# Performance work log

Hardware: AMD Instinct MI355X
Metric: run time of the kernel (lower is better)

## Reference

```python
import jax, jax.numpy as jnp
import numpy as np

MIN_NORM = 1e-15
BALL_EPS = 0.004  # torch.float32 entry of BALL_EPS
SCALING = float(np.tanh(1.0 / 2.0))  # tanh(tau/2), tau=1.0
N_GRAPHS = 512
BN_EPS = 1e-5


def _cmin(v):
    return jnp.maximum(v, MIN_NORM)


def project(x):
    norm = _cmin(jnp.linalg.norm(x, axis=-1, keepdims=True))
    maxnorm = 1.0 - BALL_EPS
    return jnp.where(norm > maxnorm, x / norm * maxnorm, x)


def isometric_transform(x, a):
    r2 = jnp.sum(a * a, axis=-1, keepdims=True) - 1.0
    u = x - a
    return r2 / _cmin(jnp.sum(u * u, axis=-1, keepdims=True)) * u + a


def reflect_at_zero(x, mu):
    a = mu / _cmin(jnp.sum(mu * mu, axis=-1, keepdims=True))
    return isometric_transform(x, a)


def reflect_through_zero(p, q, x):
    p_ = p / _cmin(jnp.linalg.norm(p, axis=-1, keepdims=True))
    q_ = q / _cmin(jnp.linalg.norm(q, axis=-1, keepdims=True))
    r = q_ - p_
    m = jnp.sum(r * x, axis=-1, keepdims=True) / jnp.sum(r * r, axis=-1, keepdims=True)
    return x - 2.0 * r * m


def logmap0(y):
    yn = _cmin(jnp.linalg.norm(y, axis=-1, keepdims=True))
    return y / yn * jnp.arctanh(jnp.clip(yn, -1.0 + 1e-15, 1.0 - 1e-15))


def unique_rows(m):
    # Emulates torch.unique(dim=0, return_inverse=True) for all-distinct rows
    # (true w.p. 1 for continuous activations): lexicographic sort, col 0 primary.
    n = m.shape[0]
    perm = jnp.lexsort(m.T[::-1])
    inv = jnp.zeros(n, jnp.int32).at[perm].set(jnp.arange(n, dtype=jnp.int32))
    return m[perm], inv


def _forward(x, edge_index, batch, W0, b0, convW1, convb1, gamma, beta, convW2,
             convb2, fc1W, fc1b, fc2W, fc2b, fc3W, fc3b):
    n = x.shape[0]
    d = W0.shape[1]
    x = jax.nn.relu(x @ W0 + b0)
    xs = [x]
    z = [jnp.zeros((1, d), x.dtype)]
    inv = [jnp.zeros(n, jnp.int32)]
    u, iv = unique_rows(jax.lax.stop_gradient(x))  # no_grad in original
    z.append(SCALING * project(u))
    inv.append(iv)
    src, dst = edge_index[0], edge_index[1]
    n_layers = convW1.shape[0]
    p_vec = jnp.zeros((d,), x.dtype).at[-1].set(1.0)
    for i in range(n_layers):
        # GINConv (eps=0): MLP(x + sum_{j->i} x_j)
        agg = jax.ops.segment_sum(x[src], dst, num_segments=n)
        h = x + agg
        h = jax.nn.relu(h @ convW1[i] + convb1[i])
        mu = jnp.mean(h, axis=0)
        var = jnp.var(h, axis=0)  # biased, as BatchNorm1d training mode
        h = gamma[i] * (h - mu) / jnp.sqrt(var + BN_EPS) + beta[i]
        x = jax.nn.relu(h @ convW2[i] + convb2[i])
        x = x.at[:, -1].set(0.0)  # x @ diag zeroes last column
        xs.append(x)
        u_full, iv = unique_rows(jax.lax.stop_gradient(jnp.concatenate(xs, axis=1)))
        cnt = jax.ops.segment_sum(jnp.ones(n, jnp.int32), iv, num_segments=n)
        u = u_full[:, -d:]
        z_children = SCALING * project(u)
        t1 = jax.ops.segment_sum(inv[i + 1], iv, num_segments=n) // cnt
        z_current = z[i + 1][t1]
        t2 = jax.ops.segment_sum(inv[i], iv, num_segments=n) // cnt
        z_parent = z[i][t2]
        z_parent = reflect_at_zero(z_parent, z_current)
        z_children = reflect_through_zero(z_parent, p_vec, z_children)
        z_all = reflect_at_zero(z_children, z_current)
        inv.append(iv)
        z.append(z_all)
    xh = logmap0(z[-1])[inv[-1]]
    out = jax.ops.segment_sum(xh, batch, num_segments=N_GRAPHS)
    out = jax.nn.relu(out @ fc1W + fc1b)
    out = jax.nn.relu(out @ fc2W + fc2b)
    out = out @ fc3W + fc3b
    return jax.nn.log_softmax(out, axis=1)


def setup_inputs() -> dict:
    N, E, D_IN, D, L, C = 50000, 800000, 128, 64, 3, 10
    key = jax.random.key(0)
    ks = jax.random.split(key, 12)
    s = 0.05
    return {
        "x": jax.random.normal(ks[0], (N, D_IN), jnp.float32),
        "edge_index": jax.random.randint(ks[1], (2, E), 0, N),
        "batch": jnp.sort(jax.random.randint(ks[2], (N,), 0, 512)),
        "W0": jax.random.normal(ks[3], (D_IN, D), jnp.float32) * s,
        "b0": jnp.zeros((D,), jnp.float32),
        "convW1": jax.random.normal(ks[4], (L, D, D), jnp.float32) * s,
        "convb1": jnp.zeros((L, D), jnp.float32),
        "gamma": jnp.ones((L, D), jnp.float32),
        "beta": jnp.zeros((L, D), jnp.float32),
        "convW2": jax.random.normal(ks[5], (L, D, D), jnp.float32) * s,
        "convb2": jnp.zeros((L, D), jnp.float32),
        "fc1W": jax.random.normal(ks[6], (D, 128), jnp.float32) * s,
        "fc1b": jnp.zeros((128,), jnp.float32),
        "fc2W": jax.random.normal(ks[7], (128, 64), jnp.float32) * s,
        "fc2b": jnp.zeros((64,), jnp.float32),
        "fc3W": jax.random.normal(ks[8], (64, C), jnp.float32) * s,
        "fc3b": jnp.zeros((C,), jnp.float32),
    }


def reference(x, edge_index, batch, W0, b0, convW1, convb1, gamma, beta, convW2,
              convb2, fc1W, fc1b, fc2W, fc2b, fc3W, fc3b):
    return _forward(x, edge_index, batch, W0, b0, convW1, convb1, gamma, beta,
                    convW2, convb2, fc1W, fc1b, fc2W, fc2b, fc3W, fc3b)
```

## Files before the change

### kernel.cpp

```cpp
#include <hip/hip_runtime.h>
#include <hip/hip_fp16.h>
#include <math.h>

#define SCALING_F 0.46211715726000974f
#define MAXNORM_F 0.996f
#define MINNORM_F 1e-15f
#define BN_EPS_F  1e-5f

#define NBUCKET 32

typedef _Float16 v8h __attribute__((ext_vector_type(8)));
typedef float    v4f __attribute__((ext_vector_type(4)));

__device__ __forceinline__ float rsum16(float v) {
  v += __shfl_xor(v, 1, 64);
  v += __shfl_xor(v, 2, 64);
  v += __shfl_xor(v, 4, 64);
  v += __shfl_xor(v, 8, 64);
  return v;
}

__device__ __forceinline__ void rsum16x6(float& a, float& b, float& c,
                                         float& d, float& e, float& f) {
#pragma unroll
  for (int o = 1; o <= 8; o <<= 1) {
    a += __shfl_xor(a, o, 64);
    b += __shfl_xor(b, o, 64);
    c += __shfl_xor(c, o, 64);
    d += __shfl_xor(d, o, 64);
    e += __shfl_xor(e, o, 64);
    f += __shfl_xor(f, o, 64);
  }
}

__device__ __forceinline__ float h2f(float v) {
  return __half2float(__float2half(v));
}

__device__ __forceinline__ void acc8(float* a, uint4 u) {
  __half2 h0 = *(__half2*)&u.x;
  __half2 h1 = *(__half2*)&u.y;
  __half2 h2 = *(__half2*)&u.z;
  __half2 h3 = *(__half2*)&u.w;
  a[0] += __low2float(h0); a[1] += __high2float(h0);
  a[2] += __low2float(h1); a[3] += __high2float(h1);
  a[4] += __low2float(h2); a[5] += __high2float(h2);
  a[6] += __low2float(h3); a[7] += __high2float(h3);
}

__device__ __forceinline__ void load4f(const __half* p, float* a) {
  uint2 u = *(const uint2*)p;
  __half2 h0 = *(__half2*)&u.x;
  __half2 h1 = *(__half2*)&u.y;
  a[0] = __low2float(h0); a[1] = __high2float(h0);
  a[2] = __low2float(h1); a[3] = __high2float(h1);
}

__global__ __launch_bounds__(256) void k_wcvt(
    const float* __restrict__ W0, const float* __restrict__ cW1,
    const float* __restrict__ cW2, int L,
    __half* __restrict__ W0T, __half* __restrict__ W1T, __half* __restrict__ W2T)
{
  int id = blockIdx.x * 256 + threadIdx.x;
  if (id < 64 * 128) {
    int n = id >> 7, k = id & 127;
    W0T[id] = __float2half(W0[(size_t)k * 64 + n]);
  }
  if (id < L * 64 * 64) {
    int l = id >> 12, rem = id & 4095;
    int n = rem >> 6, k = rem & 63;
    W1T[id] = __float2half(cW1[(size_t)l * 4096 + k * 64 + n]);
    W2T[id] = __float2half(cW2[(size_t)l * 4096 + k * 64 + n]);
  }
}

__global__ __launch_bounds__(256) void k_gb(const int* __restrict__ batch,
                                            int N, int G, int* __restrict__ gstart)
{
  int r = blockIdx.x * 256 + threadIdx.x;
  if (r >= N) return;
  int b = batch[r];
  int prev = (r == 0) ? -1 : batch[r - 1];
  for (int g = prev + 1; g <= b; ++g) gstart[g] = r;
  if (r == N - 1)
    for (int g = b + 1; g <= G; ++g) gstart[g] = N;
}

__global__ __launch_bounds__(256) void k_mm0(
    const float* __restrict__ A, const __half* __restrict__ BT,
    const float* __restrict__ bias, __half* __restrict__ X, int M)
{
  const int tid  = threadIdx.x;
  const int w    = tid >> 6;
  const int lane = tid & 63;
  const int q    = lane >> 4;
  const int i    = lane & 15;
  const int rblk = blockIdx.x * 64;
  const int arow = rblk + w * 16 + i;

  v4f acc[4];
#pragma unroll
  for (int t = 0; t < 4; ++t) acc[t] = (v4f){0.f, 0.f, 0.f, 0.f};

#pragma unroll
  for (int hh = 0; hh < 4; ++hh) {
    v8h af = (v8h){0, 0, 0, 0, 0, 0, 0, 0};
    if (arow < M) {
      const float* p = &A[(size_t)arow * 128 + hh * 32 + q * 8];
      float4 fa = *(const float4*)p;
      float4 fb = *(const float4*)(p + 4);
      af[0] = (_Float16)fa.x; af[1] = (_Float16)fa.y;
      af[2] = (_Float16)fa.z; af[3] = (_Float16)fa.w;
      af[4] = (_Float16)fb.x; af[5] = (_Float16)fb.y;
      af[6] = (_Float16)fb.z; af[7] = (_Float16)fb.w;
    }
#pragma unroll
    for (int t = 0; t < 4; ++t) {
      v8h bf = *(const v8h*)&BT[(size_t)(t * 16 + i) * 128 + hh * 32 + q * 8];
      acc[t] = __builtin_amdgcn_mfma_f32_16x16x32_f16(af, bf, acc[t], 0, 0, 0);
    }
  }

#pragma unroll
  for (int j = 0; j < 4; ++j) {
    int row = rblk + w * 16 + 4 * q + j;
    if (row >= M) continue;
#pragma unroll
    for (int t = 0; t < 4; ++t)
      X[(size_t)row * 64 + i + 16 * t] =
          __float2half(fmaxf(acc[t][j] + bias[i + 16 * t], 0.f));
  }
}

__global__ __launch_bounds__(256, 6) void k_layer1(
    const __half* __restrict__ x, const int* __restrict__ rowptr,
    const unsigned short* __restrict__ csr, const __half* __restrict__ BT,
    const float* __restrict__ bias, __half* __restrict__ h,
    float* __restrict__ gstatP, int M)
{
  __shared__ __half AsH[16][80];
  const int tid  = threadIdx.x;
  const int w    = tid >> 6;
  const int lane = tid & 63;
  const int q    = lane >> 4;
  const int i    = lane & 15;
  const int g8   = lane >> 3;
  const int i8   = lane & 7;
  const int rblk = blockIdx.x * 16;

  const int r0 = rblk + w * 4 + 0;
  const int r1 = rblk + w * 4 + 1;
  const int r2 = rblk + w * 4 + 2;
  const int r3 = rblk + w * 4 + 3;
  const bool v0 = (r0 < M), v1 = (r1 < M), v2 = (r2 < M), v3 = (r3 < M);

  float a0[8] = {0.f,0.f,0.f,0.f,0.f,0.f,0.f,0.f};
  float a1[8] = {0.f,0.f,0.f,0.f,0.f,0.f,0.f,0.f};
  float a2[8] = {0.f,0.f,0.f,0.f,0.f,0.f,0.f,0.f};
  float a3[8] = {0.f,0.f,0.f,0.f,0.f,0.f,0.f,0.f};

  int c0 = 0, e0 = 0, c1 = 0, e1 = 0, c2 = 0, e2 = 0, c3 = 0, e3 = 0;
  if (v0) { c0 = rowptr[r0]; e0 = rowptr[r0 + 1]; }
  if (v1) { c1 = rowptr[r1]; e1 = rowptr[r1 + 1]; }
  if (v2) { c2 = rowptr[r2]; e2 = rowptr[r2 + 1]; }
  if (v3) { c3 = rowptr[r3]; e3 = rowptr[r3 + 1]; }

  if (v0 && g8 == 0) acc8(a0, *(const uint4*)&x[(size_t)r0 * 64 + 8 * i8]);
  if (v1 && g8 == 0) acc8(a1, *(const uint4*)&x[(size_t)r1 * 64 + 8 * i8]);
  if (v2 && g8 == 0) acc8(a2, *(const uint4*)&x[(size_t)r2 * 64 + 8 * i8]);
  if (v3 && g8 == 0) acc8(a3, *(const uint4*)&x[(size_t)r3 * 64 + 8 * i8]);

  while ((c0 + 8 <= e0) | (c1 + 8 <= e1) | (c2 + 8 <= e2) | (c3 + 8 <= e3)) {
    const bool d0 = (c0 + 8 <= e0);
    const bool d1 = (c1 + 8 <= e1);
    const bool d2 = (c2 + 8 <= e2);
    const bool d3 = (c3 + 8 <= e3);
    int n0 = 0, n1 = 0, n2 = 0, n3 = 0;
    if (d0) n0 = csr[c0 + g8];
    if (d1) n1 = csr[c1 + g8];
    if (d2) n2 = csr[c2 + g8];
    if (d3) n3 = csr[c3 + g8];
    uint4 u0, u1, u2, u3;
    if (d0) u0 = *(const uint4*)&x[(size_t)n0 * 64 + 8 * i8];
    if (d1) u1 = *(const uint4*)&x[(size_t)n1 * 64 + 8 * i8];
    if (d2) u2 = *(const uint4*)&x[(size_t)n2 * 64 + 8 * i8];
    if (d3) u3 = *(const uint4*)&x[(size_t)n3 * 64 + 8 * i8];
    if (d0) { acc8(a0, u0); c0 += 8; }
    if (d1) { acc8(a1, u1); c1 += 8; }
    if (d2) { acc8(a2, u2); c2 += 8; }
    if (d3) { acc8(a3, u3); c3 += 8; }
  }
  {
    const int rem0 = e0 - c0;
    const int rem1 = e1 - c1;
    const int rem2 = e2 - c2;
    const int rem3 = e3 - c3;
    int n0 = 0, n1 = 0, n2 = 0, n3 = 0;
    if (g8 < rem0) n0 = csr[c0 + g8];
    if (g8 < rem1) n1 = csr[c1 + g8];
    if (g8 < rem2) n2 = csr[c2 + g8];
    if (g8 < rem3) n3 = csr[c3 + g8];
    uint4 u0, u1, u2, u3;
    if (g8 < rem0) u0 = *(const uint4*)&x[(size_t)n0 * 64 + 8 * i8];
    if (g8 < rem1) u1 = *(const uint4*)&x[(size_t)n1 * 64 + 8 * i8];
    if (g8 < rem2) u2 = *(const uint4*)&x[(size_t)n2 * 64 + 8 * i8];
    if (g8 < rem3) u3 = *(const uint4*)&x[(size_t)n3 * 64 + 8 * i8];
    if (g8 < rem0) acc8(a0, u0);
    if (g8 < rem1) acc8(a1, u1);
    if (g8 < rem2) acc8(a2, u2);
    if (g8 < rem3) acc8(a3, u3);
  }

#pragma unroll
  for (int k = 0; k < 8; ++k) {
#pragma unroll
    for (int o = 8; o <= 32; o <<= 1) {
      a0[k] += __shfl_xor(a0[k], o, 64);
      a1[k] += __shfl_xor(a1[k], o, 64);
      a2[k] += __shfl_xor(a2[k], o, 64);
      a3[k] += __shfl_xor(a3[k], o, 64);
    }
  }
  if (g8 == 0) {
    __half hv[8];
#pragma unroll
    for (int k = 0; k < 8; ++k) hv[k] = __float2half(a0[k]);
    *(uint4*)&AsH[w * 4 + 0][8 * i8] = *(uint4*)hv;
#pragma unroll
    for (int k = 0; k < 8; ++k) hv[k] = __float2half(a1[k]);
    *(uint4*)&AsH[w * 4 + 1][8 * i8] = *(uint4*)hv;
#pragma unroll
    for (int k = 0; k < 8; ++k) hv[k] = __float2half(a2[k]);
    *(uint4*)&AsH[w * 4 + 2][8 * i8] = *(uint4*)hv;
#pragma unroll
    for (int k = 0; k < 8; ++k) hv[k] = __float2half(a3[k]);
    *(uint4*)&AsH[w * 4 + 3][8 * i8] = *(uint4*)hv;
  }
  __syncthreads();

  v4f acc = (v4f){0.f, 0.f, 0.f, 0.f};
#pragma unroll
  for (int hh = 0; hh < 2; ++hh) {
    v8h af = *(const v8h*)&AsH[i][hh * 32 + q * 8];
    v8h bf = *(const v8h*)&BT[(size_t)(w * 16 + i) * 64 + hh * 32 + q * 8];
    acc = __builtin_amdgcn_mfma_f32_16x16x32_f16(af, bf, acc, 0, 0, 0);
  }

  const int col = w * 16 + i;
  float s = 0.f, qq = 0.f;
#pragma unroll
  for (int j = 0; j < 4; ++j) {
    int row = rblk + 4 * q + j;
    if (row >= M) continue;
    float v = h2f(fmaxf(acc[j] + bias[col], 0.f));
    h[(size_t)row * 64 + col] = __float2half(v);
    s += v;
    qq += v * v;
  }
  s  += __shfl_xor(s, 16, 64);  qq += __shfl_xor(qq, 16, 64);
  s  += __shfl_xor(s, 32, 64);  qq += __shfl_xor(qq, 32, 64);
  if (q == 0) {
    const int bkt = (blockIdx.x & (NBUCKET - 1)) * 128;
    atomicAdd(&gstatP[bkt + col], s);
    atomicAdd(&gstatP[bkt + 64 + col], qq);
  }
}

__global__ __launch_bounds__(256) void k_layer2(
    const __half* __restrict__ A, const __half* __restrict__ BT,
    const float* __restrict__ bias,
    const float* __restrict__ gstat, const float* __restrict__ gamma,
    const float* __restrict__ beta,
    __half* __restrict__ Xout, int M)
{
  __shared__ float scl_s[64], shf_s[64];
  __shared__ float tmp[128];
  const int tid  = threadIdx.x;
  const int w    = tid >> 6;
  const int lane = tid & 63;
  const int q    = lane >> 4;
  const int i    = lane & 15;
  const int rblk = blockIdx.x * 64;
  const int arow = rblk + w * 16 + i;

  if (tid < 128) {
    float a = 0.f;
#pragma unroll
    for (int b2 = 0; b2 < NBUCKET; ++b2) a += gstat[b2 * 128 + tid];
    tmp[tid] = a;
  }
  __syncthreads();
  if (tid < 64) {
    float mu  = tmp[tid] / (float)M;
    float var = tmp[64 + tid] / (float)M - mu * mu;
    float sv  = gamma[tid] / sqrtf(var + BN_EPS_F);
    scl_s[tid] = sv;
    shf_s[tid] = beta[tid] - mu * sv;
  }
  __syncthreads();

  v4f acc[4];
#pragma unroll
  for (int t = 0; t < 4; ++t) acc[t] = (v4f){0.f, 0.f, 0.f, 0.f};
#pragma unroll
  for (int hh = 0; hh < 2; ++hh) {
    const int k0 = hh * 32 + q * 8;
    v8h af = (v8h){0, 0, 0, 0, 0, 0, 0, 0};
    {
      float hv[8] = {0,0,0,0,0,0,0,0};
      if (arow < M) {
        uint4 u = *(const uint4*)&A[(size_t)arow * 64 + k0];
        __half2 h0 = *(__half2*)&u.x;
        __half2 h1 = *(__half2*)&u.y;
        __half2 h2 = *(__half2*)&u.z;
        __half2 h3 = *(__half2*)&u.w;
        hv[0] = __low2float(h0); hv[1] = __high2float(h0);
        hv[2] = __low2float(h1); hv[3] = __high2float(h1);
        hv[4] = __low2float(h2); hv[5] = __high2float(h2);
        hv[6] = __low2float(h3); hv[7] = __high2float(h3);
      }
#pragma unroll
      for (int k = 0; k < 8; ++k)
        af[k] = (_Float16)fmaf(hv[k], scl_s[k0 + k], shf_s[k0 + k]);
    }
#pragma unroll
    for (int t = 0; t < 4; ++t) {
      v8h bf = *(const v8h*)&BT[(size_t)(t * 16 + i) * 64 + k0];
      acc[t] = __builtin_amdgcn_mfma_f32_16x16x32_f16(af, bf, acc[t], 0, 0, 0);
    }
  }

#pragma unroll
  for (int j = 0; j < 4; ++j) {
    int row = rblk + w * 16 + 4 * q + j;
    if (row >= M) continue;
#pragma unroll
    for (int t = 0; t < 4; ++t) {
      float v = fmaxf(acc[t][j] + bias[i + 16 * t], 0.f);
      if (i == 15 && t == 3) v = 0.f;
      Xout[(size_t)row * 64 + i + 16 * t] = __float2half(v);
    }
  }
}

__global__ __launch_bounds__(256) void k_zchain(
    const __half* __restrict__ X0, const __half* __restrict__ X1,
    const __half* __restrict__ X2, const __half* __restrict__ X3,
    __half* __restrict__ Xh, int M)
{
  const int tid = threadIdx.x;
  const int i   = tid & 15;
  const int row = blockIdx.x * 16 + (tid >> 4);
  const bool valid = (row < M);

  float x0[4] = {0,0,0,0}, x1[4] = {0,0,0,0}, x2[4] = {0,0,0,0}, x3[4] = {0,0,0,0};
  if (valid) {
    load4f(&X0[(size_t)row * 64 + 4 * i], x0);
    load4f(&X1[(size_t)row * 64 + 4 * i], x1);
    load4f(&X2[(size_t)row * 64 + 4 * i], x2);
    load4f(&X3[(size_t)row * 64 + 4 * i], x3);
  }

  float zc[4], zp[4] = {0.f, 0.f, 0.f, 0.f};
  {
    float sx = rsum16(x0[0]*x0[0] + x0[1]*x0[1] + x0[2]*x0[2] + x0[3]*x0[3]);
    float norm = fmaxf(sqrtf(sx), MINNORM_F);
    float s = ((norm > MAXNORM_F) ? (MAXNORM_F / norm) : 1.0f) * SCALING_F;
#pragma unroll
    for (int e = 0; e < 4; ++e) zc[e] = x0[e] * s;
  }

  const float* Xi[3] = {x1, x2, x3};
#pragma unroll
  for (int li = 0; li < 3; ++li) {
    const float* xv = Xi[li];

    float p1 = xv[0]*xv[0] + xv[1]*xv[1] + xv[2]*xv[2] + xv[3]*xv[3];
    float p2 = zc[0]*zc[0]+zc[1]*zc[1]+zc[2]*zc[2]+zc[3]*zc[3];
    float p3 = zp[0]*zp[0]+zp[1]*zp[1]+zp[2]*zp[2]+zp[3]*zp[3];
    float p4 = zp[0]*zc[0]+zp[1]*zc[1]+zp[2]*zc[2]+zp[3]*zc[3];
    float p5 = zp[0]*xv[0]+zp[1]*xv[1]+zp[2]*xv[2]+zp[3]*xv[3];
    float p6 = zc[0]*xv[0]+zc[1]*xv[1]+zc[2]*xv[2]+zc[3]*xv[3];
    rsum16x6(p1, p2, p3, p4, p5, p6);
    float zc63 = __shfl(zc[3], 15, 16);
    float zp63 = __shfl(zp[3], 15, 16);

    float nzc2 = fmaxf(p2, MINNORM_F);
    float icz  = 1.0f / nzc2;
    float na2  = p2 * icz * icz;
    float r2   = na2 - 1.0f;
    float a63  = zc63 * icz;

    float sxn = fmaxf(sqrtf(p1), MINNORM_F);
    float sc  = ((sxn > MAXNORM_F) ? (MAXNORM_F / sxn) : 1.0f) * SCALING_F;
    float Sch2   = sc * sc * p1;
    float Szp_a  = p4 * icz;
    float Sa_ch  = sc * p6 * icz;
    float Szp_ch = sc * p5;
    float Su_a   = Szp_a - na2;
    float Su2    = p3 - 2.0f * Szp_a + na2;
    float nu2    = fmaxf(Su2, MINNORM_F);
    float t1     = r2 / nu2;
    float Szp22  = fmaxf(t1*t1*Su2 + 2.0f*t1*Su_a + na2, 0.0f);
    float npn    = fmaxf(sqrtf(Szp22), MINNORM_F);
    float ipn    = 1.0f / npn;
    float zp2_63 = t1 * (zp63 - a63) + a63;
    float Szp2ch = t1 * (Szp_ch - Sa_ch) + Sa_ch;
    float rdc    = -ipn * Szp2ch;
    float rdr    = 1.0f - 2.0f*ipn*zp2_63 + ipn*ipn*Szp22;
    float m2     = 2.0f * rdc / rdr;
    float Szp2a  = t1 * Su_a + na2;
    float Srr_a  = a63 - ipn * Szp2a;
    float Sc2a   = Sa_ch - m2 * Srr_a;
    float Sc22   = Sch2 - 2.0f*m2*rdc + m2*m2*rdr;
    float Sc2ma  = Sc22 - 2.0f*Sc2a + na2;
    float nu22   = fmaxf(Sc2ma, MINNORM_F);
    float t2     = r2 / nu22;

    float zn[4];
#pragma unroll
    for (int e = 0; e < 4; ++e) {
      float ai  = zc[e] * icz;
      float zp2 = t1 * (zp[e] - ai) + ai;
      float rri = ((i == 15 && e == 3) ? 1.0f : 0.0f) - ipn * zp2;
      float c2  = sc * xv[e] - m2 * rri;
      zn[e]     = t2 * (c2 - ai) + ai;
    }
#pragma unroll
    for (int e = 0; e < 4; ++e) { zp[e] = zc[e]; zc[e] = zn[e]; }
  }

  {
    float sz = rsum16(zc[0]*zc[0] + zc[1]*zc[1] + zc[2]*zc[2] + zc[3]*zc[3]);
    float yn  = fmaxf(sqrtf(sz), MINNORM_F);
    float t   = fminf(yn, 1.0f);
    float ath = 0.5f * logf((1.0f + t) / (1.0f - t));
    float wsc = ath / yn;
    if (valid) {
      __half hv[4];
      hv[0] = __float2half(zc[0] * wsc);
      hv[1] = __float2half(zc[1] * wsc);
      hv[2] = __float2half(zc[2] * wsc);
      hv[3] = __float2half(zc[3] * wsc);
      *(uint2*)&Xh[(size_t)row * 64 + 4 * i] = *(uint2*)hv;
    }
  }
}

__global__ __launch_bounds__(256) void k_deg(const int* __restrict__ dst, int E, int* deg) {
  int i0 = (blockIdx.x * 256 + threadIdx.x) * 4;
  if (i0 + 4 <= E) {
    int4 d = *(const int4*)&dst[i0];
    atomicAdd(&deg[d.x], 1);
    atomicAdd(&deg[d.y], 1);
    atomicAdd(&deg[d.z], 1);
    atomicAdd(&deg[d.w], 1);
  } else {
    for (int i = i0; i < E; ++i) atomicAdd(&deg[dst[i]], 1);
  }
}

__global__ __launch_bounds__(256) void k_scan1(const int* __restrict__ deg, int N,
                                               int* rowptr, int* bsum) {
  __shared__ int s[256];
  int t = threadIdx.x;
  int i = blockIdx.x * 256 + t;
  int v = (i < N) ? deg[i] : 0;
  s[t] = v;
  __syncthreads();
  for (int d = 1; d < 256; d <<= 1) {
    int add = (t >= d) ? s[t - d] : 0;
    __syncthreads();
    s[t] += add;
    __syncthreads();
  }
  if (i < N) rowptr[i] = s[t] - v;
  if (t == 255) bsum[blockIdx.x] = s[255];
}

__global__ __launch_bounds__(256) void k_scan2(const int* __restrict__ bsum, int NB, int* boff) {
  __shared__ int s[256];
  int t = threadIdx.x;
  int v = (t < NB) ? bsum[t] : 0;
  s[t] = v;
  __syncthreads();
  for (int d = 1; d < 256; d <<= 1) {
    int add = (t >= d) ? s[t - d] : 0;
    __syncthreads();
    s[t] += add;
    __syncthreads();
  }
  boff[t] = s[t] - v;
}

__global__ __launch_bounds__(256) void k_scan3(int* rowptr, const int* __restrict__ boff,
                                               int* cursor, int N, int E) {
  int i = blockIdx.x * 256 + threadIdx.x;
  if (i < N) {
    int v = rowptr[i] + boff[blockIdx.x];
    rowptr[i] = v;
    cursor[i] = v;
  }
  if (i == 0) rowptr[N] = E;
}

__global__ __launch_bounds__(256) void k_fill(const int* __restrict__ src,
                                              const int* __restrict__ dst, int E,
                                              int* cursor, unsigned short* __restrict__ csr) {
  int i0 = (blockIdx.x * 256 + threadIdx.x) * 4;
  if (i0 + 4 <= E) {
    int4 d = *(const int4*)&dst[i0];
    int4 s = *(const int4*)&src[i0];
    int p0 = atomicAdd(&cursor[d.x], 1);
    int p1 = atomicAdd(&cursor[d.y], 1);
    int p2 = atomicAdd(&cursor[d.z], 1);
    int p3 = atomicAdd(&cursor[d.w], 1);
    csr[p0] = (unsigned short)s.x;
    csr[p1] = (unsigned short)s.y;
    csr[p2] = (unsigned short)s.z;
    csr[p3] = (unsigned short)s.w;
  } else {
    for (int i = i0; i < E; ++i) {
      int p = atomicAdd(&cursor[dst[i]], 1);
      csr[p] = (unsigned short)src[i];
    }
  }
}

__global__ __launch_bounds__(128) void k_mlp(const __half* __restrict__ Xh,
                                             const int* __restrict__ gstart,
                                             const float* __restrict__ fc1W, const float* __restrict__ fc1b,
                                             const float* __restrict__ fc2W, const float* __restrict__ fc2b,
                                             const float* __restrict__ fc3W, const float* __restrict__ fc3b,
                                             float* __restrict__ out) {
  __shared__ float p2s[2][64];
  __shared__ float p[64], o1[128], o2[64], lg[10], red[2];
  int g = blockIdx.x, t = threadIdx.x;
  int beg = gstart[g], end = gstart[g + 1];
  {
    int half = t >> 6, c = t & 63;
    float a = 0.f;
    int r = beg + half;
    for (; r + 6 <= end; r += 8) {
      float v0 = __half2float(Xh[(size_t)(r + 0) * 64 + c]);
      float v1 = __half2float(Xh[(size_t)(r + 2) * 64 + c]);
      float v2 = __half2float(Xh[(size_t)(r + 4) * 64 + c]);
      float v3 = __half2float(Xh[(size_t)(r + 6) * 64 + c]);
      a += (v0 + v1) + (v2 + v3);
    }
    for (; r < end; r += 2) a += __half2float(Xh[(size_t)r * 64 + c]);
    p2s[half][c] = a;
  }
  __syncthreads();
  if (t < 64) p[t] = p2s[0][t] + p2s[1][t];
  __syncthreads();
  {
    float a = fc1b[t];
    for (int k = 0; k < 64; ++k) a = fmaf(p[k], fc1W[k * 128 + t], a);
    o1[t] = fmaxf(a, 0.f);
  }
  __syncthreads();
  if (t < 64) {
    float a = fc2b[t];
    for (int k = 0; k < 128; ++k) a = fmaf(o1[k], fc2W[k * 64 + t], a);
    o2[t] = fmaxf(a, 0.f);
  }
  __syncthreads();
  if (t < 10) {
    float a = fc3b[t];
    for (int k = 0; k < 64; ++k) a = fmaf(o2[k], fc3W[k * 10 + t], a);
    lg[t] = a;
  }
  __syncthreads();
  if (t == 0) {
    float mx = lg[0];
    for (int j = 1; j < 10; ++j) mx = fmaxf(mx, lg[j]);
    float s = 0.f;
    for (int j = 0; j < 10; ++j) s += expf(lg[j] - mx);
    red[0] = mx;
    red[1] = logf(s);
  }
  __syncthreads();
  if (t < 10) out[(size_t)g * 10 + t] = lg[t] - red[0] - red[1];
}

extern "C" void kernel_launch(void* const* d_in, const int* in_sizes, int n_in,
                              void* d_out, int out_size, void* d_ws, size_t ws_size,
                              hipStream_t stream) {
  const float* x_in  = (const float*)d_in[0];
  const int*   ei    = (const int*)d_in[1];
  const int*   batch = (const int*)d_in[2];
  const float* W0    = (const float*)d_in[3];
  const float* b0    = (const float*)d_in[4];
  const float* cW1   = (const float*)d_in[5];
  const float* cb1   = (const float*)d_in[6];
  const float* gamma = (const float*)d_in[7];
  const float* beta  = (const float*)d_in[8];
  const float* cW2   = (const float*)d_in[9];
  const float* cb2   = (const float*)d_in[10];
  const float* fc1W  = (const float*)d_in[11];
  const float* fc1b  = (const float*)d_in[12];
  const float* fc2W  = (const float*)d_in[13];
  const float* fc2b  = (const float*)d_in[14];
  const float* fc3W  = (const float*)d_in[15];
  const float* fc3b  = (const float*)d_in[16];
  float* out = (float*)d_out;

  const int N = in_sizes[0] / 128;
  const int E = in_sizes[1] / 2;
  const int L = in_sizes[5] / (64 * 64);
  const int G = out_size / 10;
  const int* src = ei;
  const int* dst = ei + E;

  char* ws = (char*)d_ws;
  size_t off = 0;
  auto alloc = [&](size_t bytes) -> char* {
    char* p = ws + off;
    off += (bytes + 255) & ~(size_t)255;
    return p;
  };
  __half* X0  = (__half*)alloc((size_t)N * 64 * 2);
  __half* X1  = (__half*)alloc((size_t)N * 64 * 2);
  __half* X2  = (__half*)alloc((size_t)N * 64 * 2);
  __half* X3  = (__half*)alloc((size_t)N * 64 * 2);
  __half* Bf  = (__half*)alloc((size_t)N * 64 * 2);
  __half* Xh  = (__half*)alloc((size_t)N * 64 * 2);
  __half* W0T = (__half*)alloc((size_t)64 * 128 * 2);
  __half* W1T = (__half*)alloc((size_t)L * 64 * 64 * 2);
  __half* W2T = (__half*)alloc((size_t)L * 64 * 64 * 2);
  int*    gstart = (int*)alloc((size_t)(G + 1) * 4);
  int*   deg  = (int*)alloc((size_t)N * 4);
  float* gstatAll = (float*)alloc((size_t)3 * NBUCKET * 128 * 4);
  char*  zero_end = ws + off;
  int*   rowptr = (int*)alloc((size_t)(N + 1) * 4);
  int*   cursor = (int*)alloc((size_t)N * 4);
  unsigned short* csr = (unsigned short*)alloc((size_t)E * 2);
  int*   bsum   = (int*)alloc(256 * 4);
  int*   boff   = (int*)alloc(256 * 4);
  __half* Xs[4] = {X0, X1, X2, X3};

  hipMemsetAsync(deg, 0, (size_t)(zero_end - (char*)deg), stream);

  const int mmGrid    = (N + 63) / 64;
  const int l1Grid    = (N + 15) / 16;
  const int zcGrid    = (N + 15) / 16;
  const int edge4Grid = (E / 4 + 255) / 256 + 1;
  const int wcvtGrid  = (((L * 4096 > 8192) ? L * 4096 : 8192) + 255) / 256;

  k_wcvt<<<wcvtGrid, 256, 0, stream>>>(W0, cW1, cW2, L, W0T, W1T, W2T);
  k_gb<<<(N + 255) / 256, 256, 0, stream>>>(batch, N, G, gstart);

  k_mm0<<<mmGrid, 256, 0, stream>>>(x_in, W0T, b0, X0, N);

  k_deg<<<edge4Grid, 256, 0, stream>>>(dst, E, deg);
  const int NB = (N + 255) / 256;
  k_scan1<<<NB, 256, 0, stream>>>(deg, N, rowptr, bsum);
  k_scan2<<<1, 256, 0, stream>>>(bsum, NB, boff);
  k_scan3<<<NB, 256, 0, stream>>>(rowptr, boff, cursor, N, E);
  k_fill<<<edge4Grid, 256, 0, stream>>>(src, dst, E, cursor, csr);

  for (int i = 0; i < L; ++i) {
    float* gstat = gstatAll + (size_t)i * NBUCKET * 128;
    k_layer1<<<l1Grid, 256, 0, stream>>>(Xs[i], rowptr, csr,
                                         W1T + (size_t)i * 4096, cb1 + i * 64,
                                         Bf, gstat, N);
    k_layer2<<<mmGrid, 256, 0, stream>>>(Bf, W2T + (size_t)i * 4096, cb2 + i * 64,
                                         gstat, gamma + i * 64, beta + i * 64,
                                         Xs[i + 1], N);
  }

  k_zchain<<<zcGrid, 256, 0, stream>>>(X0, X1, X2, X3, Xh, N);

  k_mlp<<<G, 128, 0, stream>>>(Xh, gstart, fc1W, fc1b, fc2W, fc2b, fc3W, fc3b, out);
}
```

Baseline: 360.5 us.

## Fuse front kernels, fold memset into weight conversion, unroll gather by 16

Merges the degree-count, first matmul and graph-boundary kernels into one launch that branches on block index, and does the workspace zeroing inside the weight-conversion kernel instead of a separate memset. The GIN neighbour gather loop now handles 16 neighbours per iteration, with an 8-wide remainder step, to keep more loads in flight, and the occupancy hint for k_layer1 drops from 6 to 4. The aim is fewer launches and more memory-level parallelism in the gather, at the cost of higher register pressure and a grid-stride zeroing loop inside a small kernel.

Measured after the change: 359.9 us. No clear change (-0.2%).

```diff
diff --git a/kernel.cpp b/kernel.cpp
--- a/kernel.cpp
+++ b/kernel.cpp
@@ -59,7 +59,8 @@
 __global__ __launch_bounds__(256) void k_wcvt(
     const float* __restrict__ W0, const float* __restrict__ cW1,
     const float* __restrict__ cW2, int L,
-    __half* __restrict__ W0T, __half* __restrict__ W1T, __half* __restrict__ W2T)
+    __half* __restrict__ W0T, __half* __restrict__ W1T, __half* __restrict__ W2T,
+    int* __restrict__ zbase, int zwords)
 {
   int id = blockIdx.x * 256 + threadIdx.x;
   if (id < 64 * 128) {
@@ -72,67 +73,91 @@
     W1T[id] = __float2half(cW1[(size_t)l * 4096 + k * 64 + n]);
     W2T[id] = __float2half(cW2[(size_t)l * 4096 + k * 64 + n]);
   }
-}
-
-__global__ __launch_bounds__(256) void k_gb(const int* __restrict__ batch,
-                                            int N, int G, int* __restrict__ gstart)
+  const int stride = gridDim.x * 256;
+  for (int z = id; z < zwords; z += stride) zbase[z] = 0;
+}
+
+__global__ __launch_bounds__(256) void k_front(
+    const float* __restrict__ A, const __half* __restrict__ BT,
+    const float* __restrict__ bias, __half* __restrict__ X, int M,
+    const int* __restrict__ dst, int E, int* __restrict__ deg,
+    const int* __restrict__ batch, int G, int* __restrict__ gstart,
+    int DBLK, int MBLK)
 {
-  int r = blockIdx.x * 256 + threadIdx.x;
-  if (r >= N) return;
-  int b = batch[r];
-  int prev = (r == 0) ? -1 : batch[r - 1];
-  for (int g = prev + 1; g <= b; ++g) gstart[g] = r;
-  if (r == N - 1)
-    for (int g = b + 1; g <= G; ++g) gstart[g] = N;
-}
-
-__global__ __launch_bounds__(256) void k_mm0(
-    const float* __restrict__ A, const __half* __restrict__ BT,
-    const float* __restrict__ bias, __half* __restrict__ X, int M)
-{
-  const int tid  = threadIdx.x;
-  const int w    = tid >> 6;
-  const int lane = tid & 63;
-  const int q    = lane >> 4;
-  const int i    = lane & 15;
-  const int rblk = blockIdx.x * 64;
-  const int arow = rblk + w * 16 + i;
-
-  v4f acc[4];
-#pragma unroll
-  for (int t = 0; t < 4; ++t) acc[t] = (v4f){0.f, 0.f, 0.f, 0.f};
-
-#pragma unroll
-  for (int hh = 0; hh < 4; ++hh) {
-    v8h af = (v8h){0, 0, 0, 0, 0, 0, 0, 0};
-    if (arow < M) {
-      const float* p = &A[(size_t)arow * 128 + hh * 32 + q * 8];
-      float4 fa = *(const float4*)p;
-      float4 fb = *(const float4*)(p + 4);
-      af[0] = (_Float16)fa.x; af[1] = (_Float16)fa.y;
-      af[2] = (_Float16)fa.z; af[3] = (_Float16)fa.w;
-      af[4] = (_Float16)fb.x; af[5] = (_Float16)fb.y;
-      af[6] = (_Float16)fb.z; af[7] = (_Float16)fb.w;
-    }
-#pragma unroll
-    for (int t = 0; t < 4; ++t) {
-      v8h bf = *(const v8h*)&BT[(size_t)(t * 16 + i) * 128 + hh * 32 + q * 8];
-      acc[t] = __builtin_amdgcn_mfma_f32_16x16x32_f16(af, bf, acc[t], 0, 0, 0);
-    }
-  }
-
-#pragma unroll
-  for (int j = 0; j < 4; ++j) {
-    int row = rblk + w * 16 + 4 * q + j;
-    if (row >= M) continue;
-#pragma unroll
-    for (int t = 0; t < 4; ++t)
-      X[(size_t)row * 64 + i + 16 * t] =
-          __float2half(fmaxf(acc[t][j] + bias[i + 16 * t], 0.f));
-  }
-}
-
-__global__ __launch_bounds__(256, 6) void k_layer1(
+  int bx = blockIdx.x;
+  const int tid = threadIdx.x;
+
+  if (bx < DBLK) {
+    int i0 = (bx * 256 + tid) * 4;
+    if (i0 + 4 <= E) {
+      int4 d = *(const int4*)&dst[i0];
+      atomicAdd(&deg[d.x], 1);
+      atomicAdd(&deg[d.y], 1);
+      atomicAdd(&deg[d.z], 1);
+      atomicAdd(&deg[d.w], 1);
+    } else {
+      for (int i = i0; i < E; ++i) atomicAdd(&deg[dst[i]], 1);
+    }
+    return;
+  }
+  bx -= DBLK;
+
+  if (bx < MBLK) {
+    const int w    = tid >> 6;
+    const int lane = tid & 63;
+    const int q    = lane >> 4;
+    const int i    = lane & 15;
+    const int rblk = bx * 64;
+    const int arow = rblk + w * 16 + i;
+
+    v4f acc[4];
+#pragma unroll
+    for (int t = 0; t < 4; ++t) acc[t] = (v4f){0.f, 0.f, 0.f, 0.f};
+
+#pragma unroll
+    for (int hh = 0; hh < 4; ++hh) {
+      v8h af = (v8h){0, 0, 0, 0, 0, 0, 0, 0};
+      if (arow < M) {
+        const float* p = &A[(size_t)arow * 128 + hh * 32 + q * 8];
+        float4 fa = *(const float4*)p;
+        float4 fb = *(const float4*)(p + 4);
+        af[0] = (_Float16)fa.x; af[1] = (_Float16)fa.y;
+        af[2] = (_Float16)fa.z; af[3] = (_Float16)fa.w;
+        af[4] = (_Float16)fb.x; af[5] = (_Float16)fb.y;
+        af[6] = (_Float16)fb.z; af[7] = (_Float16)fb.w;
+      }
+#pragma unroll
+      for (int t = 0; t < 4; ++t) {
+        v8h bf = *(const v8h*)&BT[(size_t)(t * 16 + i) * 128 + hh * 32 + q * 8];
+        acc[t] = __builtin_amdgcn_mfma_f32_16x16x32_f16(af, bf, acc[t], 0, 0, 0);
+      }
+    }
+
+#pragma unroll
+    for (int j = 0; j < 4; ++j) {
+      int row = rblk + w * 16 + 4 * q + j;
+      if (row >= M) continue;
+#pragma unroll
+      for (int t = 0; t < 4; ++t)
+        X[(size_t)row * 64 + i + 16 * t] =
+            __float2half(fmaxf(acc[t][j] + bias[i + 16 * t], 0.f));
+    }
+    return;
+  }
+  bx -= MBLK;
+
+  {
+    int r = bx * 256 + tid;
+    if (r >= M) return;
+    int b = batch[r];
+    int prev = (r == 0) ? -1 : batch[r - 1];
+    for (int g = prev + 1; g <= b; ++g) gstart[g] = r;
+    if (r == M - 1)
+      for (int g = b + 1; g <= G; ++g) gstart[g] = M;
+  }
+}
+
+__global__ __launch_bounds__(256, 4) void k_layer1(
     const __half* __restrict__ x, const int* __restrict__ rowptr,
     const unsigned short* __restrict__ csr, const __half* __restrict__ BT,
     const float* __restrict__ bias, __half* __restrict__ h,
@@ -170,7 +195,32 @@
   if (v2 && g8 == 0) acc8(a2, *(const uint4*)&x[(size_t)r2 * 64 + 8 * i8]);
   if (v3 && g8 == 0) acc8(a3, *(const uint4*)&x[(size_t)r3 * 64 + 8 * i8]);
 
-  while ((c0 + 8 <= e0) | (c1 + 8 <= e1) | (c2 + 8 <= e2) | (c3 + 8 <= e3)) {
+  while ((c0 + 16 <= e0) | (c1 + 16 <= e1) | (c2 + 16 <= e2) | (c3 + 16 <= e3)) {
+    const bool d0 = (c0 + 16 <= e0);
+    const bool d1 = (c1 + 16 <= e1);
+    const bool d2 = (c2 + 16 <= e2);
+    const bool d3 = (c3 + 16 <= e3);
+    int n0a = 0, n0b = 0, n1a = 0, n1b = 0;
+    int n2a = 0, n2b = 0, n3a = 0, n3b = 0;
+    if (d0) { n0a = csr[c0 + g8]; n0b = csr[c0 + 8 + g8]; }
+    if (d1) { n1a = csr[c1 + g8]; n1b = csr[c1 + 8 + g8]; }
+    if (d2) { n2a = csr[c2 + g8]; n2b = csr[c2 + 8 + g8]; }
+    if (d3) { n3a = csr[c3 + g8]; n3b = csr[c3 + 8 + g8]; }
+    uint4 u0a, u0b, u1a, u1b, u2a, u2b, u3a, u3b;
+    if (d0) { u0a = *(const uint4*)&x[(size_t)n0a * 64 + 8 * i8];
+              u0b = *(const uint4*)&x[(size_t)n0b * 64 + 8 * i8]; }
+    if (d1) { u1a = *(const uint4*)&x[(size_t)n1a * 64 + 8 * i8];
+              u1b = *(const uint4*)&x[(size_t)n1b * 64 + 8 * i8]; }
+    if (d2) { u2a = *(const uint4*)&x[(size_t)n2a * 64 + 8 * i8];
+              u2b = *(const uint4*)&x[(size_t)n2b * 64 + 8 * i8]; }
+    if (d3) { u3a = *(const uint4*)&x[(size_t)n3a * 64 + 8 * i8];
+              u3b = *(const uint4*)&x[(size_t)n3b * 64 + 8 * i8]; }
+    if (d0) { acc8(a0, u0a); acc8(a0, u0b); c0 += 16; }
+    if (d1) { acc8(a1, u1a); acc8(a1, u1b); c1 += 16; }
+    if (d2) { acc8(a2, u2a); acc8(a2, u2b); c2 += 16; }
+    if (d3) { acc8(a3, u3a); acc8(a3, u3b); c3 += 16; }
+  }
+  {
     const bool d0 = (c0 + 8 <= e0);
     const bool d1 = (c1 + 8 <= e1);
     const bool d2 = (c2 + 8 <= e2);
@@ -444,19 +494,6 @@
       hv[3] = __float2half(zc[3] * wsc);
       *(uint2*)&Xh[(size_t)row * 64 + 4 * i] = *(uint2*)hv;
     }
-  }
-}
-
-__global__ __launch_bounds__(256) void k_deg(const int* __restrict__ dst, int E, int* deg) {
-  int i0 = (blockIdx.x * 256 + threadIdx.x) * 4;
-  if (i0 + 4 <= E) {
-    int4 d = *(const int4*)&dst[i0];
-    atomicAdd(&deg[d.x], 1);
-    atomicAdd(&deg[d.y], 1);
-    atomicAdd(&deg[d.z], 1);
-    atomicAdd(&deg[d.w], 1);
-  } else {
-    for (int i = i0; i < E; ++i) atomicAdd(&deg[dst[i]], 1);
   }
 }
 
@@ -640,20 +677,24 @@
   int*   boff   = (int*)alloc(256 * 4);
   __half* Xs[4] = {X0, X1, X2, X3};
 
-  hipMemsetAsync(deg, 0, (size_t)(zero_end - (char*)deg), stream);
+  const int zwords = (int)((zero_end - (char*)deg) / 4);
 
   const int mmGrid    = (N + 63) / 64;
   const int l1Grid    = (N + 15) / 16;
   const int zcGrid    = (N + 15) / 16;
   const int edge4Grid = (E / 4 + 255) / 256 + 1;
+  const int gbGrid    = (N + 255) / 256;
   const int wcvtGrid  = (((L * 4096 > 8192) ? L * 4096 : 8192) + 255) / 256;
 
-  k_wcvt<<<wcvtGrid, 256, 0, stream>>>(W0, cW1, cW2, L, W0T, W1T, W2T);
-  k_gb<<<(N + 255) / 256, 256, 0, stream>>>(batch, N, G, gstart);
-
-  k_mm0<<<mmGrid, 256, 0, stream>>>(x_in, W0T, b0, X0, N);
-
-  k_deg<<<edge4Grid, 256, 0, stream>>>(dst, E, deg);
+  k_wcvt<<<wcvtGrid, 256, 0, stream>>>(W0, cW1, cW2, L, W0T, W1T, W2T,
+                                       deg, zwords);
+
+  k_front<<<edge4Grid + mmGrid + gbGrid, 256, 0, stream>>>(
+      x_in, W0T, b0, X0, N,
+      dst, E, deg,
+      batch, G, gstart,
+      edge4Grid, mmGrid);
+
   const int NB = (N + 255) / 256;
   k_scan1<<<NB, 256, 0, stream>>>(deg, N, rowptr, bsum);
   k_scan2<<<1, 256, 0, stream>>>(bsum, NB, boff);
```
